# Kernel optimization log

Hardware: AMD Instinct MI355X
Metric: run time of the kernel (lower is better)

Reference implementation:

```python
import jax, jax.numpy as jnp
from jax import lax
import numpy as np

B, T, K = 128, 2048, 64


def setup_inputs() -> dict:
    key = jax.random.key(0)
    k_e, k_w, k_l = jax.random.split(key, 3)
    emissions = jax.random.normal(k_e, (B, T, K), dtype=jnp.float32)
    # transition weight built by the layer (Orthogonal init; random normal is fine for a math baseline)
    transition = jax.random.normal(k_w, (K, K), dtype=jnp.float32)
    # left-aligned variable-length mask, lengths in [T//2, T]
    lengths = jax.random.randint(k_l, (B,), T // 2, T + 1)
    mask = (jnp.arange(T)[None, :] < lengths[:, None]).astype(jnp.int32)
    return {"emissions": emissions, "mask": mask, "transition": transition}


def _viterbi_decode(emissions, transition, mask_bool):
    # emissions [B,T,K], transition [K,K], mask_bool [B,T]
    b, t, k = emissions.shape
    init_score = emissions[:, 0, :]  # [B,K]
    ident_bp = jnp.broadcast_to(jnp.arange(k, dtype=jnp.int32), (b, k))

    e_tm = jnp.swapaxes(emissions, 0, 1)  # [T,B,K] time-major
    m_tm = jnp.swapaxes(mask_bool, 0, 1)  # [T,B]

    def fwd_step(score, inp):
        e_t, m_t = inp  # [B,K], [B]
        cand = score[:, :, None] + transition[None, :, :]  # [B,K_prev,K_cur]
        best = jnp.max(cand, axis=1) + e_t  # [B,K]
        bp = jnp.argmax(cand, axis=1).astype(jnp.int32)  # [B,K]
        m = m_t[:, None]
        # carry scores unchanged through padded steps; identity backpointers
        return jnp.where(m, best, score), jnp.where(m, bp, ident_bp)

    final_score, bps = lax.scan(fwd_step, init_score, (e_tm[1:], m_tm[1:]))
    last_tag = jnp.argmax(final_score, axis=1).astype(jnp.int32)  # [B]

    def back_step(tag, bp):
        prev = jnp.take_along_axis(bp, tag[:, None], axis=1)[:, 0]
        return prev, prev

    _, tags_head = lax.scan(back_step, last_tag, bps, reverse=True)  # [T-1,B]
    tags = jnp.concatenate([tags_head, last_tag[None, :]], axis=0)  # [T,B]
    tags = jnp.swapaxes(tags, 0, 1)  # [B,T]
    # tf.ragged.boolean_mask -> here: dense, padded positions zeroed
    return jnp.where(mask_bool, tags, 0)


def reference(emissions, mask, transition):
    mask_bool = mask.astype(bool)
    return _viterbi_decode(emissions, transition, mask_bool)
```

## Files before the change

### kernel.cpp

```cpp
#include <hip/hip_runtime.h>

#define BB 128
#define TT 2048
#define KK 64
#define K2S 32
#define K2W 4

__device__ __forceinline__ float max3f(float a, float b, float c) {
    return fmaxf(fmaxf(a, b), c);
}

__device__ __forceinline__ int find_len(const int* mask, int b, int lane) {
    int len = TT;
#pragma unroll 1
    for (int c = 0; c < TT / 64; ++c) {
        int m = mask[b * TT + c * 64 + lane];
        unsigned long long z = __ballot(m == 0);
        if (z) { len = c * 64 + (__ffsll(z) - 1); break; }
    }
    return len;
}

__global__ __launch_bounds__(64) __attribute__((amdgpu_waves_per_eu(1, 1)))
void vit_fwd(const float* __restrict__ em, const int* __restrict__ mask,
             const float* __restrict__ trans, float* __restrict__ sarr)
{
    __shared__ __align__(16) float sv[KK];
    const int b = blockIdx.x;
    const int lane = threadIdx.x;
    const float* emb = em + (size_t)b * TT * KK;
    float* sb = sarr + (size_t)b * TT * KK;

    float tcol[KK];
#pragma unroll
    for (int i = 0; i < KK; ++i) tcol[i] = trans[i * KK + lane];
#pragma unroll
    for (int i = 0; i < KK; ++i) asm volatile("" : "+v"(tcol[i]));

    const int lenm1 = find_len(mask, b, lane) - 1;

    float score = emb[lane];
    sb[lane] = score;
    sv[lane] = score;

    auto step = [&](float e, int tu) {
        const float4* svq = (const float4*)sv;
        float c[KK];
#pragma unroll
        for (int g = 0; g < 16; ++g) {
            float4 s4 = svq[g];
            c[4*g+0] = s4.x + tcol[4*g+0];
            c[4*g+1] = s4.y + tcol[4*g+1];
            c[4*g+2] = s4.z + tcol[4*g+2];
            c[4*g+3] = s4.w + tcol[4*g+3];
        }
        float m1[22];
#pragma unroll
        for (int g = 0; g < 21; ++g) m1[g] = max3f(c[3*g], c[3*g+1], c[3*g+2]);
        m1[21] = c[63];
        float m2[8];
#pragma unroll
        for (int g = 0; g < 7; ++g) m2[g] = max3f(m1[3*g], m1[3*g+1], m1[3*g+2]);
        m2[7] = m1[21];
        float m3a = max3f(m2[0], m2[1], m2[2]);
        float m3b = max3f(m2[3], m2[4], m2[5]);
        float m3c = fmaxf(m2[6], m2[7]);
        float best = max3f(m3a, m3b, m3c);
        score = best + e;
        sv[lane] = score;
        sb[(size_t)tu * KK + lane] = score;
    };

    float ebuf[4];
#pragma unroll
    for (int k = 0; k < 4; ++k) {
        int tp = 1 + k; if (tp > TT - 1) tp = TT - 1;
        ebuf[k] = emb[tp * KK + lane];
    }

    int t = 1;
#pragma unroll 1
    for (; t + 3 <= lenm1; t += 4) {
#pragma unroll
        for (int u = 0; u < 4; ++u) {
            float e = ebuf[u];
            int tp = t + 4 + u; if (tp > TT - 1) tp = TT - 1;
            ebuf[u] = emb[tp * KK + lane];
            step(e, t + u);
        }
    }
#pragma unroll 1
    for (; t <= lenm1; ++t) {
        float e = emb[t * KK + lane];
        step(e, t);
    }
}

__global__ __launch_bounds__(64 * K2W)
void vit_bp(const float* __restrict__ sarr, const float* __restrict__ trans,
            unsigned char* __restrict__ bp)
{
    __shared__ __align__(16) float sv[K2W][KK];
    const int b = blockIdx.x / K2S;
    const int sl = blockIdx.x % K2S;
    const int wave = threadIdx.x >> 6;
    const int lane = threadIdx.x & 63;
    const float* sb = sarr + (size_t)b * TT * KK;
    unsigned char* bpb = bp + (size_t)b * TT * KK;

    float tcol[KK];
#pragma unroll
    for (int i = 0; i < KK; ++i) tcol[i] = trans[i * KK + lane];
#pragma unroll
    for (int i = 0; i < KK; ++i) asm volatile("" : "+v"(tcol[i]));

    const int widx = sl * K2W + wave;
    float* svw = sv[wave];
    const float4* svq = (const float4*)svw;

#pragma unroll 1
    for (int t = 1 + widx; t < TT; t += K2S * K2W) {
        svw[lane] = sb[(size_t)(t - 1) * KK + lane];
        float best; int bpi;
        {
            float4 q = svq[0];
            best = q.x + tcol[0]; bpi = 0;
            float c1 = q.y + tcol[1]; bool k1_ = c1 > best; best = k1_ ? c1 : best; bpi = k1_ ? 1 : bpi;
            float c2 = q.z + tcol[2]; bool k2_ = c2 > best; best = k2_ ? c2 : best; bpi = k2_ ? 2 : bpi;
            float c3 = q.w + tcol[3]; bool k3_ = c3 > best; best = k3_ ? c3 : best; bpi = k3_ ? 3 : bpi;
        }
#pragma unroll
        for (int g = 1; g < 16; ++g) {
            float4 q = svq[g];
            float c0 = q.x + tcol[4*g+0]; bool k0 = c0 > best; best = k0 ? c0 : best; bpi = k0 ? 4*g+0 : bpi;
            float c1 = q.y + tcol[4*g+1]; bool k1_ = c1 > best; best = k1_ ? c1 : best; bpi = k1_ ? 4*g+1 : bpi;
            float c2 = q.z + tcol[4*g+2]; bool k2_ = c2 > best; best = k2_ ? c2 : best; bpi = k2_ ? 4*g+2 : bpi;
            float c3 = q.w + tcol[4*g+3]; bool k3_ = c3 > best; best = k3_ ? c3 : best; bpi = k3_ ? 4*g+3 : bpi;
        }
        bpb[(size_t)t * KK + lane] = (unsigned char)bpi;
    }
}

__global__ __launch_bounds__(64)
void vit_bt(const float* __restrict__ sarr, const int* __restrict__ mask,
            const unsigned char* __restrict__ bp, int* __restrict__ out)
{
    const int b = blockIdx.x;
    const int lane = threadIdx.x;
    const float* sb = sarr + (size_t)b * TT * KK;
    const unsigned char* bpb = bp + (size_t)b * TT * KK;
    int* outb = out + (size_t)b * TT;

    const int lenm1 = find_len(mask, b, lane) - 1;

    float bv = sb[(size_t)lenm1 * KK + lane];
    int bi = lane;
#pragma unroll
    for (int off = 32; off; off >>= 1) {
        float ov = __shfl_xor(bv, off, 64);
        int oi = __shfl_xor(bi, off, 64);
        bool take = (ov > bv) || ((ov == bv) && (oi < bi));
        bv = take ? ov : bv;
        bi = take ? oi : bi;
    }
    int tag = __builtin_amdgcn_readfirstlane(bi);

    const int cbase_top = lenm1 & ~63;
#pragma unroll 1
    for (int t0 = cbase_top + 64; t0 < TT; t0 += 64) outb[t0 + lane] = 0;

    const int rsub = lane >> 2;
    const int boff = (lane & 3) * 16;
    uint4 cur[4], nxt[4];
#pragma unroll
    for (int q = 0; q < 4; ++q)
        cur[q] = *(const uint4*)(bpb + (size_t)(cbase_top + 16 * q + rsub) * 64 + boff);
#pragma unroll
    for (int q = 0; q < 4; ++q) nxt[q] = cur[q];

    int stage = 0;
#pragma unroll 1
    for (int cbase = cbase_top; cbase >= 0; cbase -= 64) {
        if (cbase >= 64) {
#pragma unroll
            for (int q = 0; q < 4; ++q)
                nxt[q] = *(const uint4*)(bpb + (size_t)(cbase - 64 + 16 * q + rsub) * 64 + boff);
        }
#pragma unroll
        for (int s = 63; s >= 0; --s) {
            const int row = cbase + s;
            if (row <= lenm1) {
                stage = (lane == s) ? tag : stage;
                if (row >= 1) {
                    const int q = s >> 4;
                    const int lanei = ((s & 15) << 2) | (tag >> 4);
                    int w0 = __builtin_amdgcn_readlane((int)cur[q].x, lanei);
                    int w1 = __builtin_amdgcn_readlane((int)cur[q].y, lanei);
                    int w2 = __builtin_amdgcn_readlane((int)cur[q].z, lanei);
                    int w3 = __builtin_amdgcn_readlane((int)cur[q].w, lanei);
                    int a0 = (tag & 4) ? w1 : w0;
                    int a1 = (tag & 4) ? w3 : w2;
                    int word = (tag & 8) ? a1 : a0;
                    tag = (word >> ((tag & 3) * 8)) & 0xFF;
                }
            }
        }
        outb[cbase + lane] = stage;
        stage = 0;
#pragma unroll
        for (int q = 0; q < 4; ++q) cur[q] = nxt[q];
    }
}

__device__ __forceinline__ float rlane_f(float v, int lane) {
    return __int_as_float(__builtin_amdgcn_readlane(__float_as_int(v), lane));
}
__device__ __forceinline__ void cmb3(float av, int ai, float bv, int bi,
                                     float cv, int ci, float& ov, int& oi) {
    float m = fmaxf(fmaxf(av, bv), cv);
    int tbc = (bv == m) ? bi : ci;
    oi = (av == m) ? ai : tbc;
    ov = m;
}

__global__ __launch_bounds__(64) __attribute__((amdgpu_waves_per_eu(1, 1)))
void viterbi64(const float* __restrict__ em, const int* __restrict__ mask,
               const float* __restrict__ trans, int* __restrict__ out,
               unsigned char* __restrict__ bp)
{
    const int b = blockIdx.x;
    const int lane = threadIdx.x;
    const float* emb = em + (size_t)b * TT * KK;
    unsigned char* bpb = bp + (size_t)b * TT * KK;
    int* outb = out + (size_t)b * TT;

    float tcol[KK];
#pragma unroll
    for (int i = 0; i < KK; ++i) tcol[i] = trans[i * KK + lane];
#pragma unroll
    for (int i = 0; i < KK; ++i) asm volatile("" : "+v"(tcol[i]));

    const int lenm1 = find_len(mask, b, lane) - 1;
    float score = emb[lane];

    auto step = [&](float e, int tu) {
        float gv[8]; int gi[8];
#pragma unroll
        for (int g = 0; g < 8; ++g) {
            const int B8 = 8 * g;
            float c0 = rlane_f(score, B8 + 0) + tcol[B8 + 0];
            float c1 = rlane_f(score, B8 + 1) + tcol[B8 + 1];
            float c2 = rlane_f(score, B8 + 2) + tcol[B8 + 2];
            float c3 = rlane_f(score, B8 + 3) + tcol[B8 + 3];
            float c4 = rlane_f(score, B8 + 4) + tcol[B8 + 4];
            float c5 = rlane_f(score, B8 + 5) + tcol[B8 + 5];
            float c6 = rlane_f(score, B8 + 6) + tcol[B8 + 6];
            float c7 = rlane_f(score, B8 + 7) + tcol[B8 + 7];
            float a;  int ai;  cmb3(c0, B8 + 0, c1, B8 + 1, c2, B8 + 2, a, ai);
            float bb_; int bi_; cmb3(c3, B8 + 3, c4, B8 + 4, c5, B8 + 5, bb_, bi_);
            bool tk = c7 > c6;
            float dv = tk ? c7 : c6;
            int   di = tk ? (B8 + 7) : (B8 + 6);
            cmb3(a, ai, bb_, bi_, dv, di, gv[g], gi[g]);
        }
        float x; int xi; cmb3(gv[0], gi[0], gv[1], gi[1], gv[2], gi[2], x, xi);
        float y; int yi; cmb3(gv[3], gi[3], gv[4], gi[4], gv[5], gi[5], y, yi);
        bool t2 = gv[7] > gv[6];
        float z = t2 ? gv[7] : gv[6];
        int  zi = t2 ? gi[7] : gi[6];
        float best; int bpi; cmb3(x, xi, y, yi, z, zi, best, bpi);
        bpb[(size_t)tu * KK + lane] = (unsigned char)bpi;
        score = best + e;
    };

    float ebuf[4];
#pragma unroll
    for (int k = 0; k < 4; ++k) {
        int tp = 1 + k; if (tp > TT - 1) tp = TT - 1;
        ebuf[k] = emb[tp * KK + lane];
    }
    int t = 1;
#pragma unroll 1
    for (; t + 3 <= lenm1; t += 4) {
#pragma unroll
        for (int u = 0; u < 4; ++u) {
            float e = ebuf[u];
            int tp = t + 4 + u; if (tp > TT - 1) tp = TT - 1;
            ebuf[u] = emb[tp * KK + lane];
            step(e, t + u);
        }
    }
#pragma unroll 1
    for (; t <= lenm1; ++t) { float e = emb[t * KK + lane]; step(e, t); }

    float bv = score; int bi = lane;
#pragma unroll
    for (int off = 32; off; off >>= 1) {
        float ov = __shfl_xor(bv, off, 64);
        int oi = __shfl_xor(bi, off, 64);
        bool take = (ov > bv) || ((ov == bv) && (oi < bi));
        bv = take ? ov : bv;
        bi = take ? oi : bi;
    }
    int tag = __builtin_amdgcn_readfirstlane(bi);
    asm volatile("s_waitcnt vmcnt(0)" ::: "memory");

    const int cbase_top = lenm1 & ~63;
#pragma unroll 1
    for (int t0 = cbase_top + 64; t0 < TT; t0 += 64) outb[t0 + lane] = 0;

    const int rsub = lane >> 2;
    const int boff = (lane & 3) * 16;
    uint4 cur[4], nxt[4];
#pragma unroll
    for (int q = 0; q < 4; ++q)
        cur[q] = *(const uint4*)(bpb + (size_t)(cbase_top + 16 * q + rsub) * 64 + boff);
#pragma unroll
    for (int q = 0; q < 4; ++q) nxt[q] = cur[q];

    int stage = 0;
#pragma unroll 1
    for (int cbase = cbase_top; cbase >= 0; cbase -= 64) {
        if (cbase >= 64) {
#pragma unroll
            for (int q = 0; q < 4; ++q)
                nxt[q] = *(const uint4*)(bpb + (size_t)(cbase - 64 + 16 * q + rsub) * 64 + boff);
        }
#pragma unroll
        for (int s = 63; s >= 0; --s) {
            const int row = cbase + s;
            if (row <= lenm1) {
                stage = (lane == s) ? tag : stage;
                if (row >= 1) {
                    const int q = s >> 4;
                    const int lanei = ((s & 15) << 2) | (tag >> 4);
                    int w0 = __builtin_amdgcn_readlane((int)cur[q].x, lanei);
                    int w1 = __builtin_amdgcn_readlane((int)cur[q].y, lanei);
                    int w2 = __builtin_amdgcn_readlane((int)cur[q].z, lanei);
                    int w3 = __builtin_amdgcn_readlane((int)cur[q].w, lanei);
                    int a0 = (tag & 4) ? w1 : w0;
                    int a1 = (tag & 4) ? w3 : w2;
                    int word = (tag & 8) ? a1 : a0;
                    tag = (word >> ((tag & 3) * 8)) & 0xFF;
                }
            }
        }
        outb[cbase + lane] = stage;
        stage = 0;
#pragma unroll
        for (int q = 0; q < 4; ++q) cur[q] = nxt[q];
    }
}

extern "C" void kernel_launch(void* const* d_in, const int* in_sizes, int n_in,
                              void* d_out, int out_size, void* d_ws, size_t ws_size,
                              hipStream_t stream)
{
    const float* em    = (const float*)d_in[0];
    const int*   mask  = (const int*)d_in[1];
    const float* trans = (const float*)d_in[2];
    int* out = (int*)d_out;

    const size_t sbytes  = (size_t)BB * TT * KK * sizeof(float);
    const size_t bpbytes = (size_t)BB * TT * KK;

    if (ws_size >= sbytes + bpbytes) {
        float* sarr = (float*)d_ws;
        unsigned char* bp = (unsigned char*)d_ws + sbytes;
        vit_fwd<<<dim3(BB), dim3(64), 0, stream>>>(em, mask, trans, sarr);
        vit_bp<<<dim3(BB * K2S), dim3(64 * K2W), 0, stream>>>(sarr, trans, bp);
        vit_bt<<<dim3(BB), dim3(64), 0, stream>>>(sarr, mask, bp, out);
    } else {
        viterbi64<<<dim3(BB), dim3(64), 0, stream>>>(em, mask, trans, out,
                                                     (unsigned char*)d_ws);
    }
}
```

Before: 881.1 us.

## Fuse backpointer computation into forward pass, drop score array and bp kernel

The forward kernel now computes each backpointer directly, using an equality scan of the candidates against the max, and writes byte backpointers instead of storing the full float score history. The separate parallel backpointer kernel and the 64 MB score array are removed, and the final tag argmax moves into the forward kernel. The aim is to cut global memory traffic and a kernel launch, at the cost of adding about 63 compare/select ops per step to the latency-bound serial recurrence. The fallback kernel also switches to the LDS-based max tree plus equality scan.

```diff
diff --git a/kernel.cpp b/kernel.cpp
--- a/kernel.cpp
+++ b/kernel.cpp
@@ -3,8 +3,6 @@
 #define BB 128
 #define TT 2048
 #define KK 64
-#define K2S 32
-#define K2W 4
 
 __device__ __forceinline__ float max3f(float a, float b, float c) {
     return fmaxf(fmaxf(a, b), c);
@@ -22,14 +20,15 @@
 }
 
 __global__ __launch_bounds__(64) __attribute__((amdgpu_waves_per_eu(1, 1)))
-void vit_fwd(const float* __restrict__ em, const int* __restrict__ mask,
-             const float* __restrict__ trans, float* __restrict__ sarr)
+void vit_fwd_bp(const float* __restrict__ em, const int* __restrict__ mask,
+                const float* __restrict__ trans, unsigned char* __restrict__ bp,
+                int* __restrict__ last_tag)
 {
     __shared__ __align__(16) float sv[KK];
     const int b = blockIdx.x;
     const int lane = threadIdx.x;
     const float* emb = em + (size_t)b * TT * KK;
-    float* sb = sarr + (size_t)b * TT * KK;
+    unsigned char* bpb = bp + (size_t)b * TT * KK;
 
     float tcol[KK];
 #pragma unroll
@@ -40,7 +39,6 @@
     const int lenm1 = find_len(mask, b, lane) - 1;
 
     float score = emb[lane];
-    sb[lane] = score;
     sv[lane] = score;
 
     auto step = [&](float e, int tu) {
@@ -68,7 +66,11 @@
         float best = max3f(m3a, m3b, m3c);
         score = best + e;
         sv[lane] = score;
-        sb[(size_t)tu * KK + lane] = score;
+
+        int bpi = 63;
+#pragma unroll
+        for (int i = KK - 2; i >= 0; --i) bpi = (c[i] == best) ? i : bpi;
+        bpb[(size_t)tu * KK + lane] = (unsigned char)bpi;
     };
 
     float ebuf[4];
@@ -94,67 +96,8 @@
         float e = emb[t * KK + lane];
         step(e, t);
     }
-}
-
-__global__ __launch_bounds__(64 * K2W)
-void vit_bp(const float* __restrict__ sarr, const float* __restrict__ trans,
-            unsigned char* __restrict__ bp)
-{
-    __shared__ __align__(16) float sv[K2W][KK];
-    const int b = blockIdx.x / K2S;
-    const int sl = blockIdx.x % K2S;
-    const int wave = threadIdx.x >> 6;
-    const int lane = threadIdx.x & 63;
-    const float* sb = sarr + (size_t)b * TT * KK;
-    unsigned char* bpb = bp + (size_t)b * TT * KK;
-
-    float tcol[KK];
-#pragma unroll
-    for (int i = 0; i < KK; ++i) tcol[i] = trans[i * KK + lane];
-#pragma unroll
-    for (int i = 0; i < KK; ++i) asm volatile("" : "+v"(tcol[i]));
-
-    const int widx = sl * K2W + wave;
-    float* svw = sv[wave];
-    const float4* svq = (const float4*)svw;
-
-#pragma unroll 1
-    for (int t = 1 + widx; t < TT; t += K2S * K2W) {
-        svw[lane] = sb[(size_t)(t - 1) * KK + lane];
-        float best; int bpi;
-        {
-            float4 q = svq[0];
-            best = q.x + tcol[0]; bpi = 0;
-            float c1 = q.y + tcol[1]; bool k1_ = c1 > best; best = k1_ ? c1 : best; bpi = k1_ ? 1 : bpi;
-            float c2 = q.z + tcol[2]; bool k2_ = c2 > best; best = k2_ ? c2 : best; bpi = k2_ ? 2 : bpi;
-            float c3 = q.w + tcol[3]; bool k3_ = c3 > best; best = k3_ ? c3 : best; bpi = k3_ ? 3 : bpi;
-        }
-#pragma unroll
-        for (int g = 1; g < 16; ++g) {
-            float4 q = svq[g];
-            float c0 = q.x + tcol[4*g+0]; bool k0 = c0 > best; best = k0 ? c0 : best; bpi = k0 ? 4*g+0 : bpi;
-            float c1 = q.y + tcol[4*g+1]; bool k1_ = c1 > best; best = k1_ ? c1 : best; bpi = k1_ ? 4*g+1 : bpi;
-            float c2 = q.z + tcol[4*g+2]; bool k2_ = c2 > best; best = k2_ ? c2 : best; bpi = k2_ ? 4*g+2 : bpi;
-            float c3 = q.w + tcol[4*g+3]; bool k3_ = c3 > best; best = k3_ ? c3 : best; bpi = k3_ ? 4*g+3 : bpi;
-        }
-        bpb[(size_t)t * KK + lane] = (unsigned char)bpi;
-    }
-}
-
-__global__ __launch_bounds__(64)
-void vit_bt(const float* __restrict__ sarr, const int* __restrict__ mask,
-            const unsigned char* __restrict__ bp, int* __restrict__ out)
-{
-    const int b = blockIdx.x;
-    const int lane = threadIdx.x;
-    const float* sb = sarr + (size_t)b * TT * KK;
-    const unsigned char* bpb = bp + (size_t)b * TT * KK;
-    int* outb = out + (size_t)b * TT;
-
-    const int lenm1 = find_len(mask, b, lane) - 1;
-
-    float bv = sb[(size_t)lenm1 * KK + lane];
-    int bi = lane;
+
+    float bv = score; int bi = lane;
 #pragma unroll
     for (int off = 32; off; off >>= 1) {
         float ov = __shfl_xor(bv, off, 64);
@@ -163,7 +106,20 @@
         bv = take ? ov : bv;
         bi = take ? oi : bi;
     }
-    int tag = __builtin_amdgcn_readfirstlane(bi);
+    if (lane == 0) last_tag[b] = bi;
+}
+
+__global__ __launch_bounds__(64)
+void vit_bt(const int* __restrict__ mask, const unsigned char* __restrict__ bp,
+            const int* __restrict__ last_tag, int* __restrict__ out)
+{
+    const int b = blockIdx.x;
+    const int lane = threadIdx.x;
+    const unsigned char* bpb = bp + (size_t)b * TT * KK;
+    int* outb = out + (size_t)b * TT;
+
+    const int lenm1 = find_len(mask, b, lane) - 1;
+    int tag = last_tag[b];
 
     const int cbase_top = lenm1 & ~63;
 #pragma unroll 1
@@ -215,19 +171,13 @@
 __device__ __forceinline__ float rlane_f(float v, int lane) {
     return __int_as_float(__builtin_amdgcn_readlane(__float_as_int(v), lane));
 }
-__device__ __forceinline__ void cmb3(float av, int ai, float bv, int bi,
-                                     float cv, int ci, float& ov, int& oi) {
-    float m = fmaxf(fmaxf(av, bv), cv);
-    int tbc = (bv == m) ? bi : ci;
-    oi = (av == m) ? ai : tbc;
-    ov = m;
-}
 
 __global__ __launch_bounds__(64) __attribute__((amdgpu_waves_per_eu(1, 1)))
 void viterbi64(const float* __restrict__ em, const int* __restrict__ mask,
                const float* __restrict__ trans, int* __restrict__ out,
                unsigned char* __restrict__ bp)
 {
+    __shared__ __align__(16) float sv[KK];
     const int b = blockIdx.x;
     const int lane = threadIdx.x;
     const float* emb = em + (size_t)b * TT * KK;
@@ -242,35 +192,35 @@
 
     const int lenm1 = find_len(mask, b, lane) - 1;
     float score = emb[lane];
+    sv[lane] = score;
 
     auto step = [&](float e, int tu) {
-        float gv[8]; int gi[8];
-#pragma unroll
-        for (int g = 0; g < 8; ++g) {
-            const int B8 = 8 * g;
-            float c0 = rlane_f(score, B8 + 0) + tcol[B8 + 0];
-            float c1 = rlane_f(score, B8 + 1) + tcol[B8 + 1];
-            float c2 = rlane_f(score, B8 + 2) + tcol[B8 + 2];
-            float c3 = rlane_f(score, B8 + 3) + tcol[B8 + 3];
-            float c4 = rlane_f(score, B8 + 4) + tcol[B8 + 4];
-            float c5 = rlane_f(score, B8 + 5) + tcol[B8 + 5];
-            float c6 = rlane_f(score, B8 + 6) + tcol[B8 + 6];
-            float c7 = rlane_f(score, B8 + 7) + tcol[B8 + 7];
-            float a;  int ai;  cmb3(c0, B8 + 0, c1, B8 + 1, c2, B8 + 2, a, ai);
-            float bb_; int bi_; cmb3(c3, B8 + 3, c4, B8 + 4, c5, B8 + 5, bb_, bi_);
-            bool tk = c7 > c6;
-            float dv = tk ? c7 : c6;
-            int   di = tk ? (B8 + 7) : (B8 + 6);
-            cmb3(a, ai, bb_, bi_, dv, di, gv[g], gi[g]);
-        }
-        float x; int xi; cmb3(gv[0], gi[0], gv[1], gi[1], gv[2], gi[2], x, xi);
-        float y; int yi; cmb3(gv[3], gi[3], gv[4], gi[4], gv[5], gi[5], y, yi);
-        bool t2 = gv[7] > gv[6];
-        float z = t2 ? gv[7] : gv[6];
-        int  zi = t2 ? gi[7] : gi[6];
-        float best; int bpi; cmb3(x, xi, y, yi, z, zi, best, bpi);
+        const float4* svq = (const float4*)sv;
+        float c[KK];
+#pragma unroll
+        for (int g = 0; g < 16; ++g) {
+            float4 s4 = svq[g];
+            c[4*g+0] = s4.x + tcol[4*g+0];
+            c[4*g+1] = s4.y + tcol[4*g+1];
+            c[4*g+2] = s4.z + tcol[4*g+2];
+            c[4*g+3] = s4.w + tcol[4*g+3];
+        }
+        float m1[22];
+#pragma unroll
+        for (int g = 0; g < 21; ++g) m1[g] = max3f(c[3*g], c[3*g+1], c[3*g+2]);
+        m1[21] = c[63];
+        float m2[8];
+#pragma unroll
+        for (int g = 0; g < 7; ++g) m2[g] = max3f(m1[3*g], m1[3*g+1], m1[3*g+2]);
+        m2[7] = m1[21];
+        float best = max3f(max3f(m2[0], m2[1], m2[2]),
+                           max3f(m2[3], m2[4], m2[5]), fmaxf(m2[6], m2[7]));
+        score = best + e;
+        sv[lane] = score;
+        int bpi = 63;
+#pragma unroll
+        for (int i = KK - 2; i >= 0; --i) bpi = (c[i] == best) ? i : bpi;
         bpb[(size_t)tu * KK + lane] = (unsigned char)bpi;
-        score = best + e;
     };
 
     float ebuf[4];
@@ -361,15 +311,14 @@
     const float* trans = (const float*)d_in[2];
     int* out = (int*)d_out;
 
-    const size_t sbytes  = (size_t)BB * TT * KK * sizeof(float);
     const size_t bpbytes = (size_t)BB * TT * KK;
-
-    if (ws_size >= sbytes + bpbytes) {
-        float* sarr = (float*)d_ws;
-        unsigned char* bp = (unsigned char*)d_ws + sbytes;
-        vit_fwd<<<dim3(BB), dim3(64), 0, stream>>>(em, mask, trans, sarr);
-        vit_bp<<<dim3(BB * K2S), dim3(64 * K2W), 0, stream>>>(sarr, trans, bp);
-        vit_bt<<<dim3(BB), dim3(64), 0, stream>>>(sarr, mask, bp, out);
+    const size_t tagbytes = BB * sizeof(int);
+
+    if (ws_size >= bpbytes + tagbytes) {
+        unsigned char* bp = (unsigned char*)d_ws;
+        int* last_tag = (int*)((char*)d_ws + bpbytes);
+        vit_fwd_bp<<<dim3(BB), dim3(64), 0, stream>>>(em, mask, trans, bp, last_tag);
+        vit_bt<<<dim3(BB), dim3(64), 0, stream>>>(mask, bp, last_tag, out);
     } else {
         viterbi64<<<dim3(BB), dim3(64), 0, stream>>>(em, mask, trans, out,
                                                      (unsigned char*)d_ws);
```

Result: slower. 2.036 ms (+131.1%).
